# Performance work log

Hardware: AMD Instinct MI355X
Metric: run time of the kernel (lower is better)

## Reference

```python
import jax, jax.numpy as jnp
import numpy as np

D = 1024
H = 16
HD = D // H
SCALE = HD ** -0.5


def setup_inputs() -> dict:
    key = jax.random.key(0)
    ks = jax.random.split(key, 5)
    x = jax.random.normal(ks[0], (2, 2048, D), dtype=jnp.float32)
    s = 1.0 / np.sqrt(D)
    W_qkv = jax.random.uniform(ks[1], (D, 3 * D), jnp.float32, -s, s)
    b_qkv = jax.random.uniform(ks[2], (3 * D,), jnp.float32, -s, s)
    W_out = jax.random.uniform(ks[3], (D, D), jnp.float32, -s, s)
    b_out = jax.random.uniform(ks[4], (D,), jnp.float32, -s, s)
    return {"x": x, "W_qkv": W_qkv, "b_qkv": b_qkv, "W_out": W_out, "b_out": b_out}


def reference(x, W_qkv, b_qkv, W_out, b_out):
    B, S, _ = x.shape
    qkv = x @ W_qkv + b_qkv                       # [B,S,3D]
    qkv = qkv.reshape(B, S, 3, H, HD)
    q, k, v = jnp.moveaxis(qkv, 2, 0)             # each [B,S,H,HD]
    # scores: [B,H,S,S]
    scores = jnp.einsum("bshd,bthd->bhst", q, k) * SCALE
    attn = jax.nn.softmax(scores, axis=-1)        # dropout is identity in eval mode
    out = jnp.einsum("bhst,bthd->bshd", attn, v)  # [B,S,H,HD]
    out = out.reshape(B, S, H * HD)
    return out @ W_out + b_out
```

## Files before the change

### kernel.cpp

```cpp
#include <hip/hip_runtime.h>

typedef unsigned short u16;
typedef unsigned int   u32;

using short8 = __attribute__((ext_vector_type(8))) short;
using f32x4  = __attribute__((ext_vector_type(4))) float;
using half4  = __attribute__((ext_vector_type(4))) _Float16;
using half8  = __attribute__((ext_vector_type(8))) _Float16;

#define QSCALE 0.18033688011112042f

__device__ __forceinline__ u16 f2bf(float f) {
  u32 u = __float_as_uint(f);
  return (u16)((u + 0x8000u) >> 16);
}
__device__ __forceinline__ u16 f2h(float f) {
  _Float16 h = (_Float16)f;
  return __builtin_bit_cast(u16, h);
}

__device__ __forceinline__ void gld16(const u16* g, u16* l) {
  __builtin_amdgcn_global_load_lds(
      (const __attribute__((address_space(1))) unsigned int*)g,
      (__attribute__((address_space(3))) unsigned int*)l, 16, 0, 0);
}

__global__ __launch_bounds__(256) void cvt_x(const float* __restrict__ in,
                                             u16* __restrict__ out) {
  int idx = blockIdx.x * 256 + threadIdx.x;
  float4 v = reinterpret_cast<const float4*>(in)[idx];
  ushort4 o;
  o.x = f2bf(v.x); o.y = f2bf(v.y); o.z = f2bf(v.z); o.w = f2bf(v.w);
  reinterpret_cast<ushort4*>(out)[idx] = o;
}

__global__ __launch_bounds__(256) void transpose_w(const float* __restrict__ in,
                                                   u16* __restrict__ out,
                                                   int R, int C) {
  __shared__ u32 s[32][33];
  int c0 = blockIdx.x * 32, r0 = blockIdx.y * 32;
  int j = threadIdx.x & 31, i0 = threadIdx.x >> 5;
#pragma unroll
  for (int p = 0; p < 4; ++p) {
    int i = i0 + p * 8;
    s[i][j] = f2bf(in[(size_t)(r0 + i) * C + c0 + j]);
  }
  __syncthreads();
#pragma unroll
  for (int p = 0; p < 4; ++p) {
    int jj = i0 + p * 8;
    out[(size_t)(c0 + jj) * R + r0 + j] = (u16)s[j][jj];
  }
}

template <int EPI, int MT>
__global__ __launch_bounds__(256, 3) void gemm_bt(
    const u16* __restrict__ A, const u16* __restrict__ Bt,
    const float* __restrict__ bias, float* __restrict__ c_out,
    u16* __restrict__ q_out, u16* __restrict__ k_out, u16* __restrict__ vt_out,
    int M, int N, int K) {
  __shared__ __align__(16) u16 As[32 * MT * 32];
  __shared__ __align__(16) u16 Bs[128 * 32];
  const int tid = threadIdx.x;
  const int lane = tid & 63;
  const int wv = tid >> 6;
  const int l16 = lane & 15, quad = lane >> 4;
  const int wm = wv & 1, wn = wv >> 1;
  const int bx = blockIdx.x, by = blockIdx.y;

  const u16* Ab = A + (size_t)by * (32 * MT) * K;
  const u16* Bb = Bt + (size_t)bx * 128 * K;

  const f32x4 fzero = {0.0f, 0.0f, 0.0f, 0.0f};
  f32x4 acc[MT][4];
#pragma unroll
  for (int i = 0; i < MT; ++i)
#pragma unroll
    for (int j = 0; j < 4; ++j) acc[i][j] = fzero;

  for (int k0 = 0; k0 < K; k0 += 32) {
    __syncthreads();
#pragma unroll
    for (int p = 0; p < MT / 2; ++p) {
      int id = p * 256 + tid;
      int row = id >> 2, blk = id & 3;
      int gc = k0 + ((blk ^ (row & 3)) << 3);
      gld16(Ab + (size_t)row * K + gc, &As[id << 3]);
    }
#pragma unroll
    for (int p = 0; p < 2; ++p) {
      int id = p * 256 + tid;
      int row = id >> 2, blk = id & 3;
      int gc = k0 + ((blk ^ (row & 3)) << 3);
      gld16(Bb + (size_t)row * K + gc, &Bs[id << 3]);
    }
    __syncthreads();
    short8 af[MT], bfr[4];
#pragma unroll
    for (int mi = 0; mi < MT; ++mi) {
      int row = wm * (MT * 16) + mi * 16 + l16;
      af[mi] = *reinterpret_cast<const short8*>(&As[row * 32 + ((quad ^ (row & 3)) << 3)]);
    }
#pragma unroll
    for (int ni = 0; ni < 4; ++ni) {
      int row = wn * 64 + ni * 16 + l16;
      bfr[ni] = *reinterpret_cast<const short8*>(&Bs[row * 32 + ((quad ^ (row & 3)) << 3)]);
    }
#pragma unroll
    for (int mi = 0; mi < MT; ++mi)
#pragma unroll
      for (int ni = 0; ni < 4; ++ni)
        acc[mi][ni] = __builtin_amdgcn_mfma_f32_16x16x32_bf16(af[mi], bfr[ni], acc[mi][ni], 0, 0, 0);
  }

#pragma unroll
  for (int mi = 0; mi < MT; ++mi)
#pragma unroll
    for (int ni = 0; ni < 4; ++ni) {
      int col = bx * 128 + wn * 64 + ni * 16 + l16;
      float bv = bias[col];
      int row0 = by * (32 * MT) + wm * (MT * 16) + mi * 16 + quad * 4;
      if (EPI == 1) {
#pragma unroll
        for (int r = 0; r < 4; ++r)
          c_out[(size_t)(row0 + r) * N + col] = acc[mi][ni][r] + bv;
      } else {
        int which = col >> 10, rem = col & 1023;
        int h = rem >> 6, d = rem & 63;
        int b = row0 >> 11, sq0 = row0 & 2047;
        int bh = (b << 4) + h;
        if (which == 2) {
          ushort4 pk;
          pk.x = f2h(acc[mi][ni][0] + bv);
          pk.y = f2h(acc[mi][ni][1] + bv);
          pk.z = f2h(acc[mi][ni][2] + bv);
          pk.w = f2h(acc[mi][ni][3] + bv);
          size_t off = (size_t)bh * 131072 +
                       (((sq0 >> 2) * 16 + (d & 15)) * 16 + ((d >> 4) << 2));
          *reinterpret_cast<ushort4*>(&vt_out[off]) = pk;
        } else {
          size_t base = (size_t)(bh * 2048 + sq0) * 64 + d;
#pragma unroll
          for (int r = 0; r < 4; ++r) {
            float val = acc[mi][ni][r] + bv;
            if (which == 0) q_out[base + r * 64] = f2bf(val * QSCALE);
            else            k_out[base + r * 64] = f2bf(val);
          }
        }
      }
    }
}

__global__ __launch_bounds__(256, 3) void attn(
    const u16* __restrict__ q_buf, const u16* __restrict__ k_buf,
    const u16* __restrict__ vt_buf, u16* __restrict__ o_buf) {
  __shared__ __align__(16) float red[4][4][256];
  __shared__ float lred[4][16];

  const int tid = threadIdx.x;
  const int lane = tid & 63, w = tid >> 6;
  const int l16 = lane & 15, quad = lane >> 4;
  const int bh = blockIdx.x, q0 = blockIdx.y * 64;

  const u16* qg = q_buf + (size_t)bh * 131072 + q0 * 64;
  const u16* kp = k_buf + (size_t)bh * 131072 + (w * 16 + l16) * 64 + quad * 8;
  const u16* vp = vt_buf + (size_t)bh * 131072 + ((w * 4 + quad) * 16 + l16) * 16;

  short8 qb[4][2];
#pragma unroll
  for (int qi = 0; qi < 4; ++qi)
#pragma unroll
    for (int kk = 0; kk < 2; ++kk)
      qb[qi][kk] = *reinterpret_cast<const short8*>(
          qg + (qi * 16 + l16) * 64 + kk * 32 + quad * 8);

  const f32x4 fzero = {0.0f, 0.0f, 0.0f, 0.0f};
  f32x4 o_acc[4][4];
  float l_acc[4] = {0.f, 0.f, 0.f, 0.f};
#pragma unroll
  for (int qi = 0; qi < 4; ++qi)
#pragma unroll
    for (int nd = 0; nd < 4; ++nd) o_acc[qi][nd] = fzero;

  short8 ka[2][2];
  half8  vf[2][2];
  ka[0][0] = *reinterpret_cast<const short8*>(kp);
  ka[0][1] = *reinterpret_cast<const short8*>(kp + 32);
  vf[0][0] = *reinterpret_cast<const half8*>(vp);
  vf[0][1] = *reinterpret_cast<const half8*>(vp + 8);

#pragma unroll 2
  for (int i = 0; i < 32; ++i) {
    const int buf = i & 1, nb = buf ^ 1;
    if (i + 1 < 32) {
      const u16* kn = kp + (size_t)4096;
      const u16* vn = vp + (size_t)4096;
      ka[nb][0] = *reinterpret_cast<const short8*>(kn);
      ka[nb][1] = *reinterpret_cast<const short8*>(kn + 32);
      vf[nb][0] = *reinterpret_cast<const half8*>(vn);
      vf[nb][1] = *reinterpret_cast<const half8*>(vn + 8);
      kp = kn; vp = vn;
    }

    short8 k0 = ka[buf][0], k1 = ka[buf][1];
    half4 pa[4];
#pragma unroll
    for (int qi = 0; qi < 4; ++qi) {
      f32x4 s = __builtin_amdgcn_mfma_f32_16x16x32_bf16(k0, qb[qi][0], fzero, 0, 0, 0);
      s = __builtin_amdgcn_mfma_f32_16x16x32_bf16(k1, qb[qi][1], s, 0, 0, 0);
      float p0 = __builtin_amdgcn_exp2f(s[0]);
      float p1 = __builtin_amdgcn_exp2f(s[1]);
      float p2 = __builtin_amdgcn_exp2f(s[2]);
      float p3 = __builtin_amdgcn_exp2f(s[3]);
      l_acc[qi] += (p0 + p1) + (p2 + p3);
      pa[qi][0] = (_Float16)p0; pa[qi][1] = (_Float16)p1;
      pa[qi][2] = (_Float16)p2; pa[qi][3] = (_Float16)p3;
    }

    half4 vb0 = __builtin_shufflevector(vf[buf][0], vf[buf][0], 0, 1, 2, 3);
    half4 vb1 = __builtin_shufflevector(vf[buf][0], vf[buf][0], 4, 5, 6, 7);
    half4 vb2 = __builtin_shufflevector(vf[buf][1], vf[buf][1], 0, 1, 2, 3);
    half4 vb3 = __builtin_shufflevector(vf[buf][1], vf[buf][1], 4, 5, 6, 7);
#pragma unroll
    for (int qi = 0; qi < 4; ++qi) {
      o_acc[qi][0] = __builtin_amdgcn_mfma_f32_16x16x16f16(pa[qi], vb0, o_acc[qi][0], 0, 0, 0);
      o_acc[qi][1] = __builtin_amdgcn_mfma_f32_16x16x16f16(pa[qi], vb1, o_acc[qi][1], 0, 0, 0);
      o_acc[qi][2] = __builtin_amdgcn_mfma_f32_16x16x16f16(pa[qi], vb2, o_acc[qi][2], 0, 0, 0);
      o_acc[qi][3] = __builtin_amdgcn_mfma_f32_16x16x16f16(pa[qi], vb3, o_acc[qi][3], 0, 0, 0);
    }
  }

#pragma unroll
  for (int qi = 0; qi < 4; ++qi) {
    l_acc[qi] += __shfl_xor(l_acc[qi], 16, 64);
    l_acc[qi] += __shfl_xor(l_acc[qi], 32, 64);
  }

  const int b = bh >> 4, h = bh & 15;
#pragma unroll
  for (int qi = 0; qi < 4; ++qi) {
#pragma unroll
    for (int nd = 0; nd < 4; ++nd)
      *reinterpret_cast<f32x4*>(&red[w][nd][lane * 4]) = o_acc[qi][nd];
    if (lane < 16) lred[w][lane] = l_acc[qi];
    __syncthreads();
    f32x4 os = fzero, lv = fzero;
#pragma unroll
    for (int wp = 0; wp < 4; ++wp) {
      os += *reinterpret_cast<const f32x4*>(&red[wp][w][lane * 4]);
      lv += *reinterpret_cast<const f32x4*>(&lred[wp][quad * 4]);
    }
#pragma unroll
    for (int r = 0; r < 4; ++r) {
      int sq = q0 + qi * 16 + quad * 4 + r;
      o_buf[(size_t)(b * 2048 + sq) * 1024 + h * 64 + w * 16 + l16] =
          f2bf(os[r] / lv[r]);
    }
    __syncthreads();
  }
}

extern "C" void kernel_launch(void* const* d_in, const int* in_sizes, int n_in,
                              void* d_out, int out_size, void* d_ws, size_t ws_size,
                              hipStream_t stream) {
  (void)in_sizes; (void)n_in; (void)out_size; (void)ws_size;
  const float* x     = (const float*)d_in[0];
  const float* W_qkv = (const float*)d_in[1];
  const float* b_qkv = (const float*)d_in[2];
  const float* W_out = (const float*)d_in[3];
  const float* b_out = (const float*)d_in[4];
  float* out = (float*)d_out;

  char* ws = (char*)d_ws;
  u16* x_bf   = (u16*)(ws);
  u16* wqkv_t = (u16*)(ws + 8388608);
  u16* wout_t = (u16*)(ws + 14680064);
  u16* q_buf  = (u16*)(ws + 16777216);
  u16* k_buf  = (u16*)(ws + 25165824);
  u16* vt_buf = (u16*)(ws + 33554432);
  u16* o_bf   = (u16*)(ws + 41943040);

  cvt_x<<<4096, 256, 0, stream>>>(x, x_bf);
  transpose_w<<<dim3(96, 32), 256, 0, stream>>>(W_qkv, wqkv_t, 1024, 3072);
  transpose_w<<<dim3(32, 32), 256, 0, stream>>>(W_out, wout_t, 1024, 1024);
  gemm_bt<0, 4><<<dim3(24, 32), 256, 0, stream>>>(x_bf, wqkv_t, b_qkv, nullptr,
                                                  q_buf, k_buf, vt_buf, 4096, 3072, 1024);
  attn<<<dim3(32, 32), 256, 0, stream>>>(q_buf, k_buf, vt_buf, o_bf);
  gemm_bt<1, 2><<<dim3(8, 64), 256, 0, stream>>>(o_bf, wout_t, b_out, out,
                                                 nullptr, nullptr, nullptr, 4096, 1024, 1024);
}
```

Baseline: 188.9 us.

## Use 16x16x32 f16 MFMA for PV with plain transposed V layout

The P·V product now uses the K=32 f16 MFMA instead of two K=16 MFMAs. Each wave therefore handles 32 keys per iteration, building two score tiles and packing eight probabilities per lane, which halves the loop trip count. V is stored as a plain [d][seq] transpose, and the K row mapping is permuted so that the score MFMA outputs line up with the f16 A-operand layout. This is meant to cut MFMA instruction count and loop overhead. In exchange, V loads are no longer prefetched a step ahead and now stride by 2048 elements across d, so load latency may be less hidden.

New measurement: 254.0 us. 1.34x slower.

```diff
diff --git a/kernel.cpp b/kernel.cpp
--- a/kernel.cpp
+++ b/kernel.cpp
@@ -5,7 +5,6 @@
 
 using short8 = __attribute__((ext_vector_type(8))) short;
 using f32x4  = __attribute__((ext_vector_type(4))) float;
-using half4  = __attribute__((ext_vector_type(4))) _Float16;
 using half8  = __attribute__((ext_vector_type(8))) _Float16;
 
 #define QSCALE 0.18033688011112042f
@@ -135,9 +134,7 @@
           pk.y = f2h(acc[mi][ni][1] + bv);
           pk.z = f2h(acc[mi][ni][2] + bv);
           pk.w = f2h(acc[mi][ni][3] + bv);
-          size_t off = (size_t)bh * 131072 +
-                       (((sq0 >> 2) * 16 + (d & 15)) * 16 + ((d >> 4) << 2));
-          *reinterpret_cast<ushort4*>(&vt_out[off]) = pk;
+          *reinterpret_cast<ushort4*>(&vt_out[(size_t)bh * 131072 + d * 2048 + sq0]) = pk;
         } else {
           size_t base = (size_t)(bh * 2048 + sq0) * 64 + d;
 #pragma unroll
@@ -163,8 +160,9 @@
   const int bh = blockIdx.x, q0 = blockIdx.y * 64;
 
   const u16* qg = q_buf + (size_t)bh * 131072 + q0 * 64;
-  const u16* kp = k_buf + (size_t)bh * 131072 + (w * 16 + l16) * 64 + quad * 8;
-  const u16* vp = vt_buf + (size_t)bh * 131072 + ((w * 4 + quad) * 16 + l16) * 16;
+  const u16* kp = k_buf + (size_t)bh * 131072 +
+                  (w * 32 + ((l16 >> 2) << 3) + (l16 & 3)) * 64 + quad * 8;
+  const u16* vp = vt_buf + (size_t)bh * 131072 + l16 * 2048 + w * 32 + quad * 8;
 
   short8 qb[4][2];
 #pragma unroll
@@ -182,52 +180,55 @@
 #pragma unroll
     for (int nd = 0; nd < 4; ++nd) o_acc[qi][nd] = fzero;
 
-  short8 ka[2][2];
-  half8  vf[2][2];
+  short8 ka[2][4];
   ka[0][0] = *reinterpret_cast<const short8*>(kp);
   ka[0][1] = *reinterpret_cast<const short8*>(kp + 32);
-  vf[0][0] = *reinterpret_cast<const half8*>(vp);
-  vf[0][1] = *reinterpret_cast<const half8*>(vp + 8);
+  ka[0][2] = *reinterpret_cast<const short8*>(kp + 256);
+  ka[0][3] = *reinterpret_cast<const short8*>(kp + 288);
 
 #pragma unroll 2
-  for (int i = 0; i < 32; ++i) {
+  for (int i = 0; i < 16; ++i) {
     const int buf = i & 1, nb = buf ^ 1;
-    if (i + 1 < 32) {
-      const u16* kn = kp + (size_t)4096;
-      const u16* vn = vp + (size_t)4096;
+
+    half8 vf[4];
+#pragma unroll
+    for (int nd = 0; nd < 4; ++nd)
+      vf[nd] = *reinterpret_cast<const half8*>(vp + nd * 16 * 2048);
+
+    if (i + 1 < 16) {
+      const u16* kn = kp + 128 * 64;
       ka[nb][0] = *reinterpret_cast<const short8*>(kn);
       ka[nb][1] = *reinterpret_cast<const short8*>(kn + 32);
-      vf[nb][0] = *reinterpret_cast<const half8*>(vn);
-      vf[nb][1] = *reinterpret_cast<const half8*>(vn + 8);
-      kp = kn; vp = vn;
-    }
-
-    short8 k0 = ka[buf][0], k1 = ka[buf][1];
-    half4 pa[4];
+      ka[nb][2] = *reinterpret_cast<const short8*>(kn + 256);
+      ka[nb][3] = *reinterpret_cast<const short8*>(kn + 288);
+      kp = kn;
+    }
+
 #pragma unroll
     for (int qi = 0; qi < 4; ++qi) {
-      f32x4 s = __builtin_amdgcn_mfma_f32_16x16x32_bf16(k0, qb[qi][0], fzero, 0, 0, 0);
-      s = __builtin_amdgcn_mfma_f32_16x16x32_bf16(k1, qb[qi][1], s, 0, 0, 0);
-      float p0 = __builtin_amdgcn_exp2f(s[0]);
-      float p1 = __builtin_amdgcn_exp2f(s[1]);
-      float p2 = __builtin_amdgcn_exp2f(s[2]);
-      float p3 = __builtin_amdgcn_exp2f(s[3]);
-      l_acc[qi] += (p0 + p1) + (p2 + p3);
-      pa[qi][0] = (_Float16)p0; pa[qi][1] = (_Float16)p1;
-      pa[qi][2] = (_Float16)p2; pa[qi][3] = (_Float16)p3;
-    }
-
-    half4 vb0 = __builtin_shufflevector(vf[buf][0], vf[buf][0], 0, 1, 2, 3);
-    half4 vb1 = __builtin_shufflevector(vf[buf][0], vf[buf][0], 4, 5, 6, 7);
-    half4 vb2 = __builtin_shufflevector(vf[buf][1], vf[buf][1], 0, 1, 2, 3);
-    half4 vb3 = __builtin_shufflevector(vf[buf][1], vf[buf][1], 4, 5, 6, 7);
-#pragma unroll
-    for (int qi = 0; qi < 4; ++qi) {
-      o_acc[qi][0] = __builtin_amdgcn_mfma_f32_16x16x16f16(pa[qi], vb0, o_acc[qi][0], 0, 0, 0);
-      o_acc[qi][1] = __builtin_amdgcn_mfma_f32_16x16x16f16(pa[qi], vb1, o_acc[qi][1], 0, 0, 0);
-      o_acc[qi][2] = __builtin_amdgcn_mfma_f32_16x16x16f16(pa[qi], vb2, o_acc[qi][2], 0, 0, 0);
-      o_acc[qi][3] = __builtin_amdgcn_mfma_f32_16x16x16f16(pa[qi], vb3, o_acc[qi][3], 0, 0, 0);
-    }
+      f32x4 sA = __builtin_amdgcn_mfma_f32_16x16x32_bf16(ka[buf][0], qb[qi][0], fzero, 0, 0, 0);
+      sA = __builtin_amdgcn_mfma_f32_16x16x32_bf16(ka[buf][1], qb[qi][1], sA, 0, 0, 0);
+      f32x4 sB = __builtin_amdgcn_mfma_f32_16x16x32_bf16(ka[buf][2], qb[qi][0], fzero, 0, 0, 0);
+      sB = __builtin_amdgcn_mfma_f32_16x16x32_bf16(ka[buf][3], qb[qi][1], sB, 0, 0, 0);
+      float p0 = __builtin_amdgcn_exp2f(sA[0]);
+      float p1 = __builtin_amdgcn_exp2f(sA[1]);
+      float p2 = __builtin_amdgcn_exp2f(sA[2]);
+      float p3 = __builtin_amdgcn_exp2f(sA[3]);
+      float p4 = __builtin_amdgcn_exp2f(sB[0]);
+      float p5 = __builtin_amdgcn_exp2f(sB[1]);
+      float p6 = __builtin_amdgcn_exp2f(sB[2]);
+      float p7 = __builtin_amdgcn_exp2f(sB[3]);
+      l_acc[qi] += ((p0 + p1) + (p2 + p3)) + ((p4 + p5) + (p6 + p7));
+      half8 pa;
+      pa[0] = (_Float16)p0; pa[1] = (_Float16)p1;
+      pa[2] = (_Float16)p2; pa[3] = (_Float16)p3;
+      pa[4] = (_Float16)p4; pa[5] = (_Float16)p5;
+      pa[6] = (_Float16)p6; pa[7] = (_Float16)p7;
+#pragma unroll
+      for (int nd = 0; nd < 4; ++nd)
+        o_acc[qi][nd] = __builtin_amdgcn_mfma_f32_16x16x32_f16(pa, vf[nd], o_acc[qi][nd], 0, 0, 0);
+    }
+    vp += 128;
   }
 
 #pragma unroll
```
